# Kernel optimization log

Measured on AMD Instinct MI355X. Metric: run time of the kernel, lower is better.

## Reference

```python
import jax, jax.numpy as jnp
import numpy as np

H = 512        # hidden_layer_size
HL = 20        # hidden_lin
NC = 1         # n_cols
T = 8192       # seq_len


def _lstm_layer(x_seq, w_ih, w_hh, b_ih, b_hh):
    """Single-direction LSTM layer, PyTorch gate order (i, f, g, o).
    x_seq: [T, in_dim] -> returns hidden states [T, H]."""
    h_dim = w_hh.shape[1]
    # input projection for all timesteps at once (one big GEMM)
    xp = x_seq @ w_ih.T + (b_ih + b_hh)  # [T, 4H]

    def step(carry, xt):
        h, c = carry
        gates = xt + h @ w_hh.T  # [4H]
        i = jax.nn.sigmoid(gates[:h_dim])
        f = jax.nn.sigmoid(gates[h_dim:2 * h_dim])
        g = jnp.tanh(gates[2 * h_dim:3 * h_dim])
        o = jax.nn.sigmoid(gates[3 * h_dim:])
        c = f * c + i * g
        h = o * jnp.tanh(c)
        return (h, c), h

    init = (jnp.zeros((h_dim,), x_seq.dtype), jnp.zeros((h_dim,), x_seq.dtype))
    _, hs = jax.lax.scan(step, init, xp)
    return hs  # [T, H]


def setup_inputs() -> dict:
    key = jax.random.key(0)
    ks = jax.random.split(key, 13)
    s = 0.05
    return {
        "input_seq": jax.random.normal(ks[0], (T, NC), jnp.float32),
        # LSTM layer 0 (input_size=NC)
        "w_ih0": jax.random.normal(ks[1], (4 * H, NC), jnp.float32) * s,
        "w_hh0": jax.random.normal(ks[2], (4 * H, H), jnp.float32) * s,
        "b_ih0": jax.random.normal(ks[3], (4 * H,), jnp.float32) * s,
        "b_hh0": jax.random.normal(ks[4], (4 * H,), jnp.float32) * s,
        # LSTM layer 1 (input_size=H)
        "w_ih1": jax.random.normal(ks[5], (4 * H, H), jnp.float32) * s,
        "w_hh1": jax.random.normal(ks[6], (4 * H, H), jnp.float32) * s,
        "b_ih1": jax.random.normal(ks[7], (4 * H,), jnp.float32) * s,
        "b_hh1": jax.random.normal(ks[8], (4 * H,), jnp.float32) * s,
        # MLP head
        "w1": jax.random.normal(ks[9], (HL, H), jnp.float32) * s,
        "b1": jax.random.normal(ks[10], (HL,), jnp.float32) * s,
        "w2": jax.random.normal(ks[11], (NC, HL), jnp.float32) * s,
        "b2": jax.random.normal(ks[12], (NC,), jnp.float32) * s,
    }


def reference(input_seq, w_ih0, w_hh0, b_ih0, b_hh0,
              w_ih1, w_hh1, b_ih1, b_hh1, w1, b1, w2, b2):
    # 2-layer LSTM over the sequence (batch size 1 squeezed away)
    h1 = _lstm_layer(input_seq, w_ih0, w_hh0, b_ih0, b_hh0)  # [T, H]
    h2 = _lstm_layer(h1, w_ih1, w_hh1, b_ih1, b_hh1)         # [T, H]
    # MLP head (dropout is identity in eval mode)
    x = h2 @ w1.T + b1                                        # [T, HL]
    x = x @ w2.T + b2                                         # [T, NC]
    return x[-1:]                                             # [1, NC]
```

## Files before the change

kernel.cpp:

```cpp
#include <hip/hip_runtime.h>

#define T_SEQ 8192
#define POISON 0xAAAAAAAAu

typedef float vfloat4 __attribute__((ext_vector_type(4)));

static __device__ __forceinline__ float sigm(float x)  { return 1.0f / (1.0f + __expf(-x)); }
static __device__ __forceinline__ float tanhq(float x) { return 1.0f - 2.0f / (__expf(2.0f * x) + 1.0f); }

static __device__ __forceinline__ void sysStore4(float* p, vfloat4 v) {
  asm volatile("global_store_dwordx4 %0, %1, off sc0 sc1" :: "v"(p), "v"(v) : "memory");
}
static __device__ __forceinline__ vfloat4 pollLoad4(const float* p) {
  vfloat4 v;
  asm volatile("global_load_dwordx4 %0, %1, off sc1\n\ts_waitcnt vmcnt(0)"
               : "=v"(v) : "v"(p) : "memory");
  return v;
}
static __device__ __forceinline__ bool valid4(vfloat4 v) {
  return (__float_as_uint(v[0]) != POISON) && (__float_as_uint(v[1]) != POISON) &&
         (__float_as_uint(v[2]) != POISON) && (__float_as_uint(v[3]) != POISON);
}
static __device__ __forceinline__ vfloat4 pollRow(const float* src, int* gd) {
  __builtin_amdgcn_s_sleep(12);
  vfloat4 v;
  for (;;) {
    v = pollLoad4(src);
    if (valid4(v)) break;
    if (--(*gd) <= 0) break;
    __builtin_amdgcn_s_sleep(2);
  }
  return v;
}

#define SWZ(i) ((i) + (((i) >> 6) << 2))

#define WLIST(X) X(0) X(1) X(2) X(3) X(4) X(5) X(6) X(7) X(8) X(9) X(10) X(11) X(12) X(13) X(14) X(15)
#define DECLW(k) float4 W##k = wp4[k];
#define PINW(k)  asm volatile("" : "+v"(W##k.x), "+v"(W##k.y), "+v"(W##k.z), "+v"(W##k.w));
#define DOFMA(k) { float4 hv = hp4[k]; \
  a0 = __builtin_fmaf(W##k.x, hv.x, a0); a1 = __builtin_fmaf(W##k.y, hv.y, a1); \
  a2 = __builtin_fmaf(W##k.z, hv.z, a2); a3 = __builtin_fmaf(W##k.w, hv.w, a3); }

__global__ __launch_bounds__(256, 1) void lstm_main(
    const float* __restrict__ input_seq,
    const float* __restrict__ w_ih0, const float* __restrict__ w_hh0,
    const float* __restrict__ b_ih0, const float* __restrict__ b_hh0,
    const float* __restrict__ w_ih1, const float* __restrict__ w_hh1,
    const float* __restrict__ b_ih1, const float* __restrict__ b_hh1,
    float* __restrict__ h0buf, float* __restrict__ h1buf, int mode)
{
  __shared__ float xin[T_SEQ];
  __shared__ __align__(16) float hb[2][1088];
  __shared__ __align__(16) float hstage[8];
  const int tid  = threadIdx.x;
  const int lane = tid & 63;
  const int wv   = tid >> 6;
  const int wg   = blockIdx.x;
  const int h0s  = (mode == 2) ? 1024 : 512;
  const int h1s  = (mode == 2) ? 2048 : ((mode == 1) ? 1024 : 512);
  int gd = 1 << 22;

  if (wg < 64) {
    for (int i = tid; i < T_SEQ; i += 256) xin[i] = input_seq[i];
    const int q  = tid & 7;
    const int lr = tid >> 3;
    const int jl = lr >> 2;
    const int g  = lr & 3;
    const int grow = g * 512 + wg * 8 + jl;
    const float4* wp4 = (const float4*)(w_hh0 + (size_t)grow * 512 + q * 64);
    WLIST(DECLW)
    const float wx   = w_ih0[grow];
    const float bias = b_ih0[grow] + b_hh0[grow];
    const int hsIdx = wv * 2 + (lane >> 5);
    const int h0off = (mode == 2) ? ((tid >> 1) * 16 + (tid & 1) * 4) : (4 * tid);
    float c = 0.0f;
    __syncthreads();

    for (int t = 0; t < T_SEQ; ++t) {
      WLIST(PINW)
      float* hl = hb[t & 1];
      if (tid < 128) {
        vfloat4 v;
        if (t == 0) { v[0] = v[1] = v[2] = v[3] = 0.0f; }
        else        { v = pollRow(h0buf + (size_t)(t - 1) * h0s + h0off, &gd); }
        *(vfloat4*)&hl[SWZ(4 * tid)] = v;
      }
      __syncthreads();
      const float4* hp4 = (const float4*)(hl + q * 68);
      float a0 = 0.f, a1 = 0.f, a2 = 0.f, a3 = 0.f;
      WLIST(DOFMA)
      float acc = (a0 + a1) + (a2 + a3);
      acc += __shfl_xor(acc, 1);
      acc += __shfl_xor(acc, 2);
      acc += __shfl_xor(acc, 4);
      float pre = acc + bias + wx * xin[t];
      float pf = __shfl_xor(pre, 8);
      float pg = __shfl_xor(pre, 16);
      float po = __shfl_xor(pre, 24);
      float i_ = sigm(pre), f_ = sigm(pf), g_ = tanhq(pg), o_ = sigm(po);
      c = f_ * c + i_ * g_;
      float h = o_ * tanhq(c);
      if ((lane & 31) == 0) hstage[hsIdx] = h;
      __syncthreads();
      if (mode == 2) {
        if (tid < 4) {
          vfloat4 hv = *(vfloat4*)&hstage[(tid & 1) * 4];
          sysStore4(h0buf + (size_t)t * 1024 + wg * 16 + tid * 4, hv);
        }
      } else {
        if (tid < 2) {
          vfloat4 hv = *(vfloat4*)&hstage[4 * tid];
          sysStore4(h0buf + (size_t)t * 512 + wg * 8 + 4 * tid, hv);
        }
      }
    }
  } else {
    const int wg1 = wg - 64;
    const int q  = tid & 15;
    const int lr = tid >> 4;
    const int jl = lr >> 2;
    const int g  = lr & 3;
    const int grow = g * 512 + wg1 * 4 + jl;
    const float* wsrc = (q < 8) ? (w_ih1 + (size_t)grow * 512 + q * 64)
                                : (w_hh1 + (size_t)grow * 512 + (q - 8) * 64);
    const float4* wp4 = (const float4*)wsrc;
    WLIST(DECLW)
    const float bias = b_ih1[grow] + b_hh1[grow];
    const int blkOff = (mode == 2) ? (wg1 * 16)
                     : ((mode == 1) ? ((wg1 >> 1) * 16 + (wg1 & 1) * 4) : (wg1 * 4));
    const int chunkOff = (q < 8) ? q * 68 : 544 + (q - 8) * 68;
    const int h0off = (mode == 2) ? ((tid >> 1) * 16 + (tid & 1) * 4) : (4 * tid);
    const int p2 = tid - 128;
    const int srcOff = (mode == 2) ? (p2 * 16)
                     : ((mode == 1) ? ((p2 >> 1) * 16 + (p2 & 1) * 4) : (4 * p2));
    float c = 0.0f;
    __syncthreads();

    for (int t = 0; t < T_SEQ; ++t) {
      WLIST(PINW)
      float* hl = hb[t & 1];
      vfloat4 v;
      if (tid < 128) {
        v = pollRow(h0buf + (size_t)t * h0s + h0off, &gd);
        *(vfloat4*)&hl[SWZ(4 * tid)] = v;
      } else {
        if (t == 0) { v[0] = v[1] = v[2] = v[3] = 0.0f; }
        else        { v = pollRow(h1buf + (size_t)(t - 1) * h1s + srcOff, &gd); }
        *(vfloat4*)&hl[544 + SWZ(4 * p2)] = v;
      }
      __syncthreads();
      const float4* hp4 = (const float4*)(hl + chunkOff);
      float a0 = 0.f, a1 = 0.f, a2 = 0.f, a3 = 0.f;
      WLIST(DOFMA)
      float acc = (a0 + a1) + (a2 + a3);
      acc += __shfl_xor(acc, 1);
      acc += __shfl_xor(acc, 2);
      acc += __shfl_xor(acc, 4);
      acc += __shfl_xor(acc, 8);
      float pre = acc + bias;
      float pf = __shfl_xor(pre, 16);
      float pg = __shfl_xor(pre, 32);
      float po = __shfl_xor(pre, 48);
      float i_ = sigm(pre), f_ = sigm(pf), g_ = tanhq(pg), o_ = sigm(po);
      c = f_ * c + i_ * g_;
      float h = o_ * tanhq(c);
      if (lane == 0) hstage[wv] = h;
      __syncthreads();
      if (mode == 2) {
        if (tid < 4) {
          vfloat4 hv = *(vfloat4*)&hstage[0];
          sysStore4(h1buf + (size_t)t * 2048 + wg1 * 16 + tid * 4, hv);
        }
      } else {
        if (tid == 0) {
          vfloat4 hv = *(vfloat4*)&hstage[0];
          sysStore4(h1buf + (size_t)t * h1s + blkOff, hv);
        }
      }
    }
  }
}

__global__ void lstm_head(const float* __restrict__ h1buf,
                          const float* __restrict__ w1, const float* __restrict__ b1,
                          const float* __restrict__ w2, const float* __restrict__ b2,
                          float* __restrict__ out, int mode)
{
  const int lane = threadIdx.x;
  const int h1s = (mode == 2) ? 2048 : ((mode == 1) ? 1024 : 512);
  const float* h2 = h1buf + (size_t)(T_SEQ - 1) * h1s;
  float hv[8];
  #pragma unroll
  for (int k = 0; k < 8; ++k) {
    int jj = lane * 8 + k;
    int off = (mode == 2) ? ((jj >> 2) * 16 + (jj & 3))
            : ((mode == 1) ? (lane * 16 + k)
                           : jj);
    hv[k] = h2[off];
  }
  float o = 0.0f;
  for (int r = 0; r < 20; ++r) {
    const float* wr = w1 + r * 512 + lane * 8;
    float p = 0.0f;
    #pragma unroll
    for (int k = 0; k < 8; ++k) p += wr[k] * hv[k];
    #pragma unroll
    for (int m = 1; m < 64; m <<= 1) p += __shfl_xor(p, m);
    o += w2[r] * (p + b1[r]);
  }
  if (lane == 0) out[0] = o + b2[0];
}

extern "C" void kernel_launch(void* const* d_in, const int* in_sizes, int n_in,
                              void* d_out, int out_size, void* d_ws, size_t ws_size,
                              hipStream_t stream)
{
  const float* input_seq = (const float*)d_in[0];
  const float* w_ih0 = (const float*)d_in[1];
  const float* w_hh0 = (const float*)d_in[2];
  const float* b_ih0 = (const float*)d_in[3];
  const float* b_hh0 = (const float*)d_in[4];
  const float* w_ih1 = (const float*)d_in[5];
  const float* w_hh1 = (const float*)d_in[6];
  const float* b_ih1 = (const float*)d_in[7];
  const float* b_hh1 = (const float*)d_in[8];
  const float* w1 = (const float*)d_in[9];
  const float* b1 = (const float*)d_in[10];
  const float* w2 = (const float*)d_in[11];
  const float* b2 = (const float*)d_in[12];
  (void)in_sizes; (void)n_in; (void)out_size;

  char* ws = (char*)d_ws;
  float* h0buf = (float*)ws;
  const size_t needA = (size_t)T_SEQ * 1024 * 4 + (size_t)T_SEQ * 2048 * 4;
  const size_t needB = (size_t)T_SEQ * 512 * 4 + (size_t)T_SEQ * 1024 * 4;
  int mode;
  float* h1buf;
  if (ws_size >= needA)      { mode = 2; h1buf = (float*)(ws + (size_t)T_SEQ * 1024 * 4); }
  else if (ws_size >= needB) { mode = 1; h1buf = (float*)(ws + (size_t)T_SEQ * 512 * 4); }
  else                       { mode = 0; h1buf = (float*)(ws + (size_t)T_SEQ * 512 * 4); }

  hipLaunchKernelGGL(lstm_main, dim3(192), dim3(256), 0, stream,
                     input_seq, w_ih0, w_hh0, b_ih0, b_hh0,
                     w_ih1, w_hh1, b_ih1, b_hh1, h0buf, h1buf, mode);
  hipLaunchKernelGGL(lstm_head, dim3(1), dim3(64), 0, stream,
                     h1buf, w1, b1, w2, b2, (float*)d_out, mode);
}
```

Measured before the change: 12.08 ms.

## Fuse both LSTM layers into one wavefront-skewed persistent kernel on 64 blocks

Each of 64 blocks now computes both layers: layer 0 at step t and layer 1 at step t-1 in the same iteration, keeping all three weight matrices in registers (48 float4 per thread). This halves the number of grid-wide handoffs per step by sharing one poll/barrier round across both layers and removes the separate 128 layer-1 blocks. It also drops the initial sleep before polling. The trade-off is much higher register pressure (about 192 VGPRs of weights), a longer serial critical path per iteration, and two extra block barriers per step.

```diff
diff --git a/kernel.cpp b/kernel.cpp
--- a/kernel.cpp
+++ b/kernel.cpp
@@ -22,7 +22,6 @@
          (__float_as_uint(v[2]) != POISON) && (__float_as_uint(v[3]) != POISON);
 }
 static __device__ __forceinline__ vfloat4 pollRow(const float* src, int* gd) {
-  __builtin_amdgcn_s_sleep(12);
   vfloat4 v;
   for (;;) {
     v = pollLoad4(src);
@@ -35,14 +34,24 @@
 
 #define SWZ(i) ((i) + (((i) >> 6) << 2))
 
-#define WLIST(X) X(0) X(1) X(2) X(3) X(4) X(5) X(6) X(7) X(8) X(9) X(10) X(11) X(12) X(13) X(14) X(15)
-#define DECLW(k) float4 W##k = wp4[k];
-#define PINW(k)  asm volatile("" : "+v"(W##k.x), "+v"(W##k.y), "+v"(W##k.z), "+v"(W##k.w));
-#define DOFMA(k) { float4 hv = hp4[k]; \
-  a0 = __builtin_fmaf(W##k.x, hv.x, a0); a1 = __builtin_fmaf(W##k.y, hv.y, a1); \
-  a2 = __builtin_fmaf(W##k.z, hv.z, a2); a3 = __builtin_fmaf(W##k.w, hv.w, a3); }
-
-__global__ __launch_bounds__(256, 1) void lstm_main(
+#define WL(X) X(0) X(1) X(2) X(3) X(4) X(5) X(6) X(7) X(8) X(9) X(10) X(11) X(12) X(13) X(14) X(15)
+#define DECLA(k) float4 WA##k = wpA[k];
+#define DECLI(k) float4 WI##k = wpI[k];
+#define DECLH(k) float4 WH##k = wpH[k];
+#define PINA(k)  asm volatile("" : "+v"(WA##k.x), "+v"(WA##k.y), "+v"(WA##k.z), "+v"(WA##k.w));
+#define PINI(k)  asm volatile("" : "+v"(WI##k.x), "+v"(WI##k.y), "+v"(WI##k.z), "+v"(WI##k.w));
+#define PINH(k)  asm volatile("" : "+v"(WH##k.x), "+v"(WH##k.y), "+v"(WH##k.z), "+v"(WH##k.w));
+#define FMA_A(k) { float4 hv = hp0[k]; \
+  a0 = __builtin_fmaf(WA##k.x, hv.x, a0); a1 = __builtin_fmaf(WA##k.y, hv.y, a1); \
+  a2 = __builtin_fmaf(WA##k.z, hv.z, a2); a3 = __builtin_fmaf(WA##k.w, hv.w, a3); }
+#define FMA_I(k) { float4 hv = hp0[k]; \
+  a0 = __builtin_fmaf(WI##k.x, hv.x, a0); a1 = __builtin_fmaf(WI##k.y, hv.y, a1); \
+  a2 = __builtin_fmaf(WI##k.z, hv.z, a2); a3 = __builtin_fmaf(WI##k.w, hv.w, a3); }
+#define FMA_H(k) { float4 hv = hp1[k]; \
+  a0 = __builtin_fmaf(WH##k.x, hv.x, a0); a1 = __builtin_fmaf(WH##k.y, hv.y, a1); \
+  a2 = __builtin_fmaf(WH##k.z, hv.z, a2); a3 = __builtin_fmaf(WH##k.w, hv.w, a3); }
+
+__global__ __launch_bounds__(256, 1) void lstm_fused(
     const float* __restrict__ input_seq,
     const float* __restrict__ w_ih0, const float* __restrict__ w_hh0,
     const float* __restrict__ b_ih0, const float* __restrict__ b_hh0,
@@ -52,131 +61,105 @@
 {
   __shared__ float xin[T_SEQ];
   __shared__ __align__(16) float hb[2][1088];
-  __shared__ __align__(16) float hstage[8];
+  __shared__ __align__(16) float hstA[8];
+  __shared__ __align__(16) float hstB[8];
   const int tid  = threadIdx.x;
   const int lane = tid & 63;
   const int wv   = tid >> 6;
   const int wg   = blockIdx.x;
-  const int h0s  = (mode == 2) ? 1024 : 512;
-  const int h1s  = (mode == 2) ? 2048 : ((mode == 1) ? 1024 : 512);
+  const int hs   = (mode == 2) ? 1024 : 512;
   int gd = 1 << 22;
 
-  if (wg < 64) {
-    for (int i = tid; i < T_SEQ; i += 256) xin[i] = input_seq[i];
-    const int q  = tid & 7;
-    const int lr = tid >> 3;
-    const int jl = lr >> 2;
-    const int g  = lr & 3;
-    const int grow = g * 512 + wg * 8 + jl;
-    const float4* wp4 = (const float4*)(w_hh0 + (size_t)grow * 512 + q * 64);
-    WLIST(DECLW)
-    const float wx   = w_ih0[grow];
-    const float bias = b_ih0[grow] + b_hh0[grow];
-    const int hsIdx = wv * 2 + (lane >> 5);
-    const int h0off = (mode == 2) ? ((tid >> 1) * 16 + (tid & 1) * 4) : (4 * tid);
-    float c = 0.0f;
+  for (int i = tid; i < T_SEQ; i += 256) xin[i] = input_seq[i];
+
+  const int q  = tid & 7;
+  const int lr = tid >> 3;
+  const int jl = lr >> 2;
+  const int g  = lr & 3;
+  const int grow = g * 512 + wg * 8 + jl;
+  const float4* wpA = (const float4*)(w_hh0 + (size_t)grow * 512 + q * 64);
+  const float4* wpI = (const float4*)(w_ih1 + (size_t)grow * 512 + q * 64);
+  const float4* wpH = (const float4*)(w_hh1 + (size_t)grow * 512 + q * 64);
+  WL(DECLA) WL(DECLI) WL(DECLH)
+  const float wx    = w_ih0[grow];
+  const float biasA = b_ih0[grow] + b_hh0[grow];
+  const float biasB = b_ih1[grow] + b_hh1[grow];
+  const int hsIdx = wv * 2 + (lane >> 5);
+  const int pq  = (tid < 128) ? tid : (tid - 128);
+  const int off = (mode == 2) ? ((pq >> 1) * 16 + (pq & 1) * 4) : (4 * pq);
+  float cA = 0.0f, cB = 0.0f;
+  __syncthreads();
+
+  for (int t = 0; t <= T_SEQ; ++t) {
+    WL(PINA) WL(PINI) WL(PINH)
+    float* hl = hb[t & 1];
+    if (tid < 128) {
+      vfloat4 v;
+      if (t == 0) { v[0] = v[1] = v[2] = v[3] = 0.0f; }
+      else        { v = pollRow(h0buf + (size_t)(t - 1) * hs + off, &gd); }
+      *(vfloat4*)&hl[SWZ(4 * tid)] = v;
+    } else {
+      vfloat4 v;
+      if (t <= 1) { v[0] = v[1] = v[2] = v[3] = 0.0f; }
+      else        { v = pollRow(h1buf + (size_t)(t - 2) * hs + off, &gd); }
+      *(vfloat4*)&hl[544 + SWZ(4 * (tid - 128))] = v;
+    }
     __syncthreads();
-
-    for (int t = 0; t < T_SEQ; ++t) {
-      WLIST(PINW)
-      float* hl = hb[t & 1];
-      if (tid < 128) {
-        vfloat4 v;
-        if (t == 0) { v[0] = v[1] = v[2] = v[3] = 0.0f; }
-        else        { v = pollRow(h0buf + (size_t)(t - 1) * h0s + h0off, &gd); }
-        *(vfloat4*)&hl[SWZ(4 * tid)] = v;
-      }
-      __syncthreads();
-      const float4* hp4 = (const float4*)(hl + q * 68);
+    const float4* hp0 = (const float4*)(hl + q * 68);
+    const float4* hp1 = (const float4*)(hl + 544 + q * 68);
+
+    if (t < T_SEQ) {
       float a0 = 0.f, a1 = 0.f, a2 = 0.f, a3 = 0.f;
-      WLIST(DOFMA)
+      WL(FMA_A)
       float acc = (a0 + a1) + (a2 + a3);
       acc += __shfl_xor(acc, 1);
       acc += __shfl_xor(acc, 2);
       acc += __shfl_xor(acc, 4);
-      float pre = acc + bias + wx * xin[t];
+      float pre = acc + biasA + wx * xin[t];
       float pf = __shfl_xor(pre, 8);
       float pg = __shfl_xor(pre, 16);
       float po = __shfl_xor(pre, 24);
       float i_ = sigm(pre), f_ = sigm(pf), g_ = tanhq(pg), o_ = sigm(po);
-      c = f_ * c + i_ * g_;
-      float h = o_ * tanhq(c);
-      if ((lane & 31) == 0) hstage[hsIdx] = h;
-      __syncthreads();
+      cA = f_ * cA + i_ * g_;
+      float h = o_ * tanhq(cA);
+      if ((lane & 31) == 0) hstA[hsIdx] = h;
+    }
+    __syncthreads();
+    if (t < T_SEQ) {
       if (mode == 2) {
-        if (tid < 4) {
-          vfloat4 hv = *(vfloat4*)&hstage[(tid & 1) * 4];
-          sysStore4(h0buf + (size_t)t * 1024 + wg * 16 + tid * 4, hv);
-        }
+        if (tid < 4) sysStore4(h0buf + (size_t)t * 1024 + wg * 16 + tid * 4,
+                               *(vfloat4*)&hstA[(tid & 1) * 4]);
       } else {
-        if (tid < 2) {
-          vfloat4 hv = *(vfloat4*)&hstage[4 * tid];
-          sysStore4(h0buf + (size_t)t * 512 + wg * 8 + 4 * tid, hv);
-        }
+        if (tid < 2) sysStore4(h0buf + (size_t)t * 512 + wg * 8 + tid * 4,
+                               *(vfloat4*)&hstA[4 * tid]);
       }
     }
-  } else {
-    const int wg1 = wg - 64;
-    const int q  = tid & 15;
-    const int lr = tid >> 4;
-    const int jl = lr >> 2;
-    const int g  = lr & 3;
-    const int grow = g * 512 + wg1 * 4 + jl;
-    const float* wsrc = (q < 8) ? (w_ih1 + (size_t)grow * 512 + q * 64)
-                                : (w_hh1 + (size_t)grow * 512 + (q - 8) * 64);
-    const float4* wp4 = (const float4*)wsrc;
-    WLIST(DECLW)
-    const float bias = b_ih1[grow] + b_hh1[grow];
-    const int blkOff = (mode == 2) ? (wg1 * 16)
-                     : ((mode == 1) ? ((wg1 >> 1) * 16 + (wg1 & 1) * 4) : (wg1 * 4));
-    const int chunkOff = (q < 8) ? q * 68 : 544 + (q - 8) * 68;
-    const int h0off = (mode == 2) ? ((tid >> 1) * 16 + (tid & 1) * 4) : (4 * tid);
-    const int p2 = tid - 128;
-    const int srcOff = (mode == 2) ? (p2 * 16)
-                     : ((mode == 1) ? ((p2 >> 1) * 16 + (p2 & 1) * 4) : (4 * p2));
-    float c = 0.0f;
-    __syncthreads();
-
-    for (int t = 0; t < T_SEQ; ++t) {
-      WLIST(PINW)
-      float* hl = hb[t & 1];
-      vfloat4 v;
-      if (tid < 128) {
-        v = pollRow(h0buf + (size_t)t * h0s + h0off, &gd);
-        *(vfloat4*)&hl[SWZ(4 * tid)] = v;
-      } else {
-        if (t == 0) { v[0] = v[1] = v[2] = v[3] = 0.0f; }
-        else        { v = pollRow(h1buf + (size_t)(t - 1) * h1s + srcOff, &gd); }
-        *(vfloat4*)&hl[544 + SWZ(4 * p2)] = v;
-      }
-      __syncthreads();
-      const float4* hp4 = (const float4*)(hl + chunkOff);
+
+    if (t >= 1) {
       float a0 = 0.f, a1 = 0.f, a2 = 0.f, a3 = 0.f;
-      WLIST(DOFMA)
+      WL(FMA_I)
+      WL(FMA_H)
       float acc = (a0 + a1) + (a2 + a3);
       acc += __shfl_xor(acc, 1);
       acc += __shfl_xor(acc, 2);
       acc += __shfl_xor(acc, 4);
-      acc += __shfl_xor(acc, 8);
-      float pre = acc + bias;
-      float pf = __shfl_xor(pre, 16);
-      float pg = __shfl_xor(pre, 32);
-      float po = __shfl_xor(pre, 48);
+      float pre = acc + biasB;
+      float pf = __shfl_xor(pre, 8);
+      float pg = __shfl_xor(pre, 16);
+      float po = __shfl_xor(pre, 24);
       float i_ = sigm(pre), f_ = sigm(pf), g_ = tanhq(pg), o_ = sigm(po);
-      c = f_ * c + i_ * g_;
-      float h = o_ * tanhq(c);
-      if (lane == 0) hstage[wv] = h;
-      __syncthreads();
+      cB = f_ * cB + i_ * g_;
+      float h = o_ * tanhq(cB);
+      if ((lane & 31) == 0) hstB[hsIdx] = h;
+    }
+    __syncthreads();
+    if (t >= 1) {
       if (mode == 2) {
-        if (tid < 4) {
-          vfloat4 hv = *(vfloat4*)&hstage[0];
-          sysStore4(h1buf + (size_t)t * 2048 + wg1 * 16 + tid * 4, hv);
-        }
+        if (tid < 4) sysStore4(h1buf + (size_t)(t - 1) * 1024 + wg * 16 + tid * 4,
+                               *(vfloat4*)&hstB[(tid & 1) * 4]);
       } else {
-        if (tid == 0) {
-          vfloat4 hv = *(vfloat4*)&hstage[0];
-          sysStore4(h1buf + (size_t)t * h1s + blkOff, hv);
-        }
+        if (tid < 2) sysStore4(h1buf + (size_t)(t - 1) * 512 + wg * 8 + tid * 4,
+                               *(vfloat4*)&hstB[4 * tid]);
       }
     }
   }
@@ -188,15 +171,14 @@
                           float* __restrict__ out, int mode)
 {
   const int lane = threadIdx.x;
-  const int h1s = (mode == 2) ? 2048 : ((mode == 1) ? 1024 : 512);
+  const int h1s = (mode == 2) ? 1024 : 512;
   const float* h2 = h1buf + (size_t)(T_SEQ - 1) * h1s;
   float hv[8];
   #pragma unroll
   for (int k = 0; k < 8; ++k) {
     int jj = lane * 8 + k;
-    int off = (mode == 2) ? ((jj >> 2) * 16 + (jj & 3))
-            : ((mode == 1) ? (lane * 16 + k)
-                           : jj);
+    int off = (mode == 2) ? ((jj >> 3) * 16 + (jj & 7))
+                          : jj;
     hv[k] = h2[off];
   }
   float o = 0.0f;
@@ -233,15 +215,13 @@
 
   char* ws = (char*)d_ws;
   float* h0buf = (float*)ws;
-  const size_t needA = (size_t)T_SEQ * 1024 * 4 + (size_t)T_SEQ * 2048 * 4;
-  const size_t needB = (size_t)T_SEQ * 512 * 4 + (size_t)T_SEQ * 1024 * 4;
+  const size_t needA = (size_t)T_SEQ * 1024 * 4 * 2;
   int mode;
   float* h1buf;
-  if (ws_size >= needA)      { mode = 2; h1buf = (float*)(ws + (size_t)T_SEQ * 1024 * 4); }
-  else if (ws_size >= needB) { mode = 1; h1buf = (float*)(ws + (size_t)T_SEQ * 512 * 4); }
-  else                       { mode = 0; h1buf = (float*)(ws + (size_t)T_SEQ * 512 * 4); }
-
-  hipLaunchKernelGGL(lstm_main, dim3(192), dim3(256), 0, stream,
+  if (ws_size >= needA) { mode = 2; h1buf = (float*)(ws + (size_t)T_SEQ * 1024 * 4); }
+  else                  { mode = 0; h1buf = (float*)(ws + (size_t)T_SEQ * 512 * 4); }
+
+  hipLaunchKernelGGL(lstm_fused, dim3(64), dim3(256), 0, stream,
                      input_seq, w_ih0, w_hh0, b_ih0, b_hh0,
                      w_ih1, w_hh1, b_ih1, b_hh1, h0buf, h1buf, mode);
   hipLaunchKernelGGL(lstm_head, dim3(1), dim3(64), 0, stream,
```

Measured after the change: 26.34 ms. 118% more time.

## Prefetch layer-0 h row and overlap input-projection FMAs with recurrent poll

Applied to the files above, without the earlier changes.

In layer-1 blocks, each thread now holds half its weights from w_ih1 and half from w_hh1. The input-projection half of the dot product is computed from the already-available h0 row before waiting on the layer-1 recurrent state. The h0 row for step t+1 is prefetched into the other buffer during step t, using a poll that skips the initial sleep when the data is already there. The aim is to take the layer-0 dependency and half the FMAs off the layer-1 critical path, at the cost of a reworked weight/LDS mapping and an extra double-buffer dependency.

```diff
diff --git a/kernel.cpp b/kernel.cpp
--- a/kernel.cpp
+++ b/kernel.cpp
@@ -21,8 +21,7 @@
   return (__float_as_uint(v[0]) != POISON) && (__float_as_uint(v[1]) != POISON) &&
          (__float_as_uint(v[2]) != POISON) && (__float_as_uint(v[3]) != POISON);
 }
-static __device__ __forceinline__ vfloat4 pollRow(const float* src, int* gd) {
-  __builtin_amdgcn_s_sleep(12);
+static __device__ __forceinline__ vfloat4 pollRetry(const float* src, int* gd) {
   vfloat4 v;
   for (;;) {
     v = pollLoad4(src);
@@ -32,13 +31,33 @@
   }
   return v;
 }
+static __device__ __forceinline__ vfloat4 pollFresh(const float* src, int* gd) {
+  __builtin_amdgcn_s_sleep(12);
+  return pollRetry(src, gd);
+}
+static __device__ __forceinline__ vfloat4 pollStale(const float* src, int* gd) {
+  vfloat4 v = pollLoad4(src);
+  if (valid4(v)) return v;
+  __builtin_amdgcn_s_sleep(12);
+  return pollRetry(src, gd);
+}
 
 #define SWZ(i) ((i) + (((i) >> 6) << 2))
 
 #define WLIST(X) X(0) X(1) X(2) X(3) X(4) X(5) X(6) X(7) X(8) X(9) X(10) X(11) X(12) X(13) X(14) X(15)
-#define DECLW(k) float4 W##k = wp4[k];
+#define L8A(X) X(0) X(1) X(2) X(3) X(4) X(5) X(6) X(7)
+#define L8B(X) X(8) X(9) X(10) X(11) X(12) X(13) X(14) X(15)
+#define DECLW(k)  float4 W##k = wp4[k];
+#define DECLWI(k) float4 W##k = wpI[k];
+#define DECLWH(k) float4 W##k = wpH[(k) - 8];
 #define PINW(k)  asm volatile("" : "+v"(W##k.x), "+v"(W##k.y), "+v"(W##k.z), "+v"(W##k.w));
 #define DOFMA(k) { float4 hv = hp4[k]; \
+  a0 = __builtin_fmaf(W##k.x, hv.x, a0); a1 = __builtin_fmaf(W##k.y, hv.y, a1); \
+  a2 = __builtin_fmaf(W##k.z, hv.z, a2); a3 = __builtin_fmaf(W##k.w, hv.w, a3); }
+#define FMAA(k) { float4 hv = hpA[k]; \
+  a0 = __builtin_fmaf(W##k.x, hv.x, a0); a1 = __builtin_fmaf(W##k.y, hv.y, a1); \
+  a2 = __builtin_fmaf(W##k.z, hv.z, a2); a3 = __builtin_fmaf(W##k.w, hv.w, a3); }
+#define FMAB(k) { float4 hv = hpB[(k) - 8]; \
   a0 = __builtin_fmaf(W##k.x, hv.x, a0); a1 = __builtin_fmaf(W##k.y, hv.y, a1); \
   a2 = __builtin_fmaf(W##k.z, hv.z, a2); a3 = __builtin_fmaf(W##k.w, hv.w, a3); }
 
@@ -83,7 +102,7 @@
       if (tid < 128) {
         vfloat4 v;
         if (t == 0) { v[0] = v[1] = v[2] = v[3] = 0.0f; }
-        else        { v = pollRow(h0buf + (size_t)(t - 1) * h0s + h0off, &gd); }
+        else        { v = pollFresh(h0buf + (size_t)(t - 1) * h0s + h0off, &gd); }
         *(vfloat4*)&hl[SWZ(4 * tid)] = v;
       }
       __syncthreads();
@@ -122,37 +141,51 @@
     const int jl = lr >> 2;
     const int g  = lr & 3;
     const int grow = g * 512 + wg1 * 4 + jl;
-    const float* wsrc = (q < 8) ? (w_ih1 + (size_t)grow * 512 + q * 64)
-                                : (w_hh1 + (size_t)grow * 512 + (q - 8) * 64);
-    const float4* wp4 = (const float4*)wsrc;
-    WLIST(DECLW)
+    const float4* wpI = (const float4*)(w_ih1 + (size_t)grow * 512 + q * 32);
+    const float4* wpH = (const float4*)(w_hh1 + (size_t)grow * 512 + q * 32);
+    L8A(DECLWI) L8B(DECLWH)
     const float bias = b_ih1[grow] + b_hh1[grow];
     const int blkOff = (mode == 2) ? (wg1 * 16)
                      : ((mode == 1) ? ((wg1 >> 1) * 16 + (wg1 & 1) * 4) : (wg1 * 4));
-    const int chunkOff = (q < 8) ? q * 68 : 544 + (q - 8) * 68;
     const int h0off = (mode == 2) ? ((tid >> 1) * 16 + (tid & 1) * 4) : (4 * tid);
     const int p2 = tid - 128;
     const int srcOff = (mode == 2) ? (p2 * 16)
                      : ((mode == 1) ? ((p2 >> 1) * 16 + (p2 & 1) * 4) : (4 * p2));
+    const int cA = 32 * q + ((q >> 1) << 2);
+    const int cB = 544 + cA;
     float c = 0.0f;
+    __syncthreads();
+    if (tid < 128) {
+      vfloat4 v = pollStale(h0buf + 0 * (size_t)h0s + h0off, &gd);
+      *(vfloat4*)&hb[0][SWZ(4 * tid)] = v;
+    }
     __syncthreads();
 
     for (int t = 0; t < T_SEQ; ++t) {
       WLIST(PINW)
       float* hl = hb[t & 1];
-      vfloat4 v;
+      float* hn = hb[(t + 1) & 1];
+      const float4* hpA = (const float4*)(hl + cA);
+      float a0 = 0.f, a1 = 0.f, a2 = 0.f, a3 = 0.f;
+      L8A(FMAA)
+      asm volatile("" : "+v"(a0), "+v"(a1), "+v"(a2), "+v"(a3));
       if (tid < 128) {
-        v = pollRow(h0buf + (size_t)t * h0s + h0off, &gd);
-        *(vfloat4*)&hl[SWZ(4 * tid)] = v;
+        if (t + 1 < T_SEQ) {
+          vfloat4 v = pollStale(h0buf + (size_t)(t + 1) * h0s + h0off, &gd);
+          *(vfloat4*)&hn[SWZ(4 * tid)] = v;
+        }
       } else {
+        vfloat4 v;
         if (t == 0) { v[0] = v[1] = v[2] = v[3] = 0.0f; }
-        else        { v = pollRow(h1buf + (size_t)(t - 1) * h1s + srcOff, &gd); }
+        else {
+          __builtin_amdgcn_s_sleep(10);
+          v = pollRetry(h1buf + (size_t)(t - 1) * h1s + srcOff, &gd);
+        }
         *(vfloat4*)&hl[544 + SWZ(4 * p2)] = v;
       }
       __syncthreads();
-      const float4* hp4 = (const float4*)(hl + chunkOff);
-      float a0 = 0.f, a1 = 0.f, a2 = 0.f, a3 = 0.f;
-      WLIST(DOFMA)
+      const float4* hpB = (const float4*)(hl + cB);
+      L8B(FMAB)
       float acc = (a0 + a1) + (a2 + a3);
       acc += __shfl_xor(acc, 1);
       acc += __shfl_xor(acc, 2);
```

New measurement: 14.55 ms. 1.21x slower.
